# Kernel optimization log

Measured on AMD Instinct MI355X. Metric: run time of the kernel, lower is better.

## Reference

```python
import jax, jax.numpy as jnp
import numpy as np

B, V, H = 4, 256, 128
EPS = 1e-5


def setup_inputs() -> dict:
    key = jax.random.key(0)
    ks = jax.random.split(key, 16)
    inp = {
        "h1": jax.random.normal(ks[0], (B, V, H), jnp.float32),
        "h2": jax.random.normal(ks[1], (B, V, H), jnp.float32),
        "e": jax.random.normal(ks[2], (B, V, V, H), jnp.float32),
        "graph": jax.random.randint(ks[3], (B, V, V), 0, 2, jnp.int32),
    }
    scale = 1.0 / np.sqrt(H)
    for i, nm in enumerate(["U1", "U2", "V1", "V2", "A1", "A2", "C"]):
        inp[f"W_{nm}"] = jax.random.normal(ks[4 + i], (H, H), jnp.float32) * scale
        inp[f"b_{nm}"] = jnp.zeros((H,), jnp.float32)
    for nm in ["h1", "h2", "e"]:
        inp[f"g_{nm}"] = jnp.ones((H,), jnp.float32)   # BN gamma
        inp[f"be_{nm}"] = jnp.zeros((H,), jnp.float32)  # BN beta
    return inp


def _lin(x, W, b):
    # torch nn.Linear: x @ W.T + b
    return jnp.einsum('...i,oi->...o', x, W) + b


def _bn(x, g, b):
    # BatchNorm1d with track_running_stats=False: batch stats over flattened leading dims
    sh = x.shape
    x2 = x.reshape(-1, sh[-1])
    m = x2.mean(axis=0)
    v = x2.var(axis=0)  # biased, as torch BN uses for normalization
    return ((x2 - m) * jax.lax.rsqrt(v + EPS) * g + b).reshape(sh)


def reference(h1, h2, e, graph,
              W_U1, b_U1, W_U2, b_U2, W_V1, b_V1, W_V2, b_V2,
              W_A1, b_A1, W_A2, b_A2, W_C, b_C,
              g_h1, be_h1, g_h2, be_h2, g_e, be_e):
    h1_in, h2_in, e_in = h1, h2, e

    Uh1 = _lin(h1, W_U1, b_U1)
    Uh2 = _lin(h2, W_U2, b_U2)
    Vh1 = _lin(h1, W_V1, b_V1)
    Vh2 = _lin(h2, W_V2, b_V2)

    # Wh1[b,i,j,h] = Vh1[b,j,h] + Vh2[b,i,h] ; Wh2 = transpose(1,2) pattern
    Wh1 = Vh1[:, None, :, :] + Vh2[:, :, None, :]
    Wh2 = Vh1[:, :, None, :] + Vh2[:, None, :, :]

    Ah1 = _lin(h1, W_A1, b_A1)
    Ah2 = _lin(h2, W_A2, b_A2)
    Ce = _lin(e, W_C, b_C)
    e_new = Ah1[:, None, :, :] + Ah2[:, :, None, :] + Ce  # B x V x V x H

    gates = jax.nn.sigmoid(e_new)
    gates_T = jax.nn.sigmoid(jnp.transpose(e_new, (0, 2, 1, 3)))

    # aggregation = 'sum' over dim 2 (graph unused for sum)
    h1n = Uh1 + jnp.sum(gates * Wh1, axis=2)
    h2n = Uh2 + jnp.sum(gates_T * Wh2, axis=2)

    h1n = jax.nn.relu(_bn(h1n, g_h1, be_h1))
    h2n = jax.nn.relu(_bn(h2n, g_h2, be_h2))
    e_out = jax.nn.relu(_bn(e_new, g_e, be_e))

    # mode == 'residual'
    return (h1_in + h1n, h2_in + h2n, e_in + e_out)
```

## Files before the change

### kernel.cpp

```cpp
#include <hip/hip_runtime.h>
#include <hip/hip_fp16.h>
#include <math.h>

#define BB 4
#define VV 256
#define HH 128
#define EPS 1e-5f

typedef __attribute__((ext_vector_type(8))) short short8;
typedef __attribute__((ext_vector_type(8))) __bf16 bf16x8;
typedef __attribute__((ext_vector_type(4))) float f32x4;

__device__ __forceinline__ float sigm_(float x) {
    float ex = __builtin_amdgcn_exp2f(-1.44269504f * x);
    return __builtin_amdgcn_rcpf(1.0f + ex);
}

__device__ __forceinline__ bf16x8 as_bf(short8 s) {
    union { short8 s; bf16x8 b; } u; u.s = s; return u.b;
}

__device__ __forceinline__ void split8n(const float4 x0, const float4 x1,
                                        bf16x8& hi, bf16x8& lo) {
    float xs[8] = {x0.x, x0.y, x0.z, x0.w, x1.x, x1.y, x1.z, x1.w};
    #pragma unroll
    for (int i = 0; i < 8; ++i) {
        float x = xs[i];
        __bf16 h = (__bf16)x;
        float r = x - (float)h;
        hi[i] = h;
        lo[i] = (__bf16)r;
    }
}

__global__ __launch_bounds__(256) void k0_splitW(const float* __restrict__ W_C,
                                                 short* __restrict__ Whl) {
    int t = blockIdx.x * 256 + threadIdx.x;
    int lane = t & 63;
    int grp = t >> 6;
    int kstep = grp >> 3, nsub = grp & 7;
    int n = (lane & 15) * 8 + nsub;
    int kb = kstep * 32 + ((lane >> 4) & 3) * 8;
    const float4* src = (const float4*)(W_C + (size_t)n * HH + kb);
    float4 x0 = src[0], x1 = src[1];
    bf16x8 hi, lo;
    split8n(x0, x1, hi, lo);
    union { bf16x8 b; short8 s; } uh, ul;
    uh.b = hi; ul.b = lo;
    short8* dst = (short8*)Whl;
    dst[(size_t)grp * 128 + 0 * 64 + lane] = uh.s;
    dst[(size_t)grp * 128 + 1 * 64 + lane] = ul.s;
}

struct LinArgs {
    const float* x1; const float* x2;
    const float* W[6]; const float* b[6]; const float* b2[6];
    float* out[6]; float* outf[6];
};

__global__ __launch_bounds__(128) void k1_linears(LinArgs a) {
    __shared__ float xs[2][8][HH];
    const int t = threadIdx.x;
    const int r0 = blockIdx.x * 8;
    {
        const float4* s1 = (const float4*)(a.x1 + (size_t)r0 * HH);
        const float4* s2 = (const float4*)(a.x2 + (size_t)r0 * HH);
        float4* d1 = (float4*)&xs[0][0][0];
        float4* d2 = (float4*)&xs[1][0][0];
        #pragma unroll
        for (int p = 0; p < 2; ++p) {
            d1[t + p * 128] = s1[t + p * 128];
            d2[t + p * 128] = s2[t + p * 128];
        }
    }
    __syncthreads();
    const int h = t;
    const int l15h = h >> 3, nsh = h & 7;
    for (int g = 0; g < 6; ++g) {
        const float* W = a.W[g];
        const float (*x)[HH] = (g < 3) ? xs[0] : xs[1];
        float acc[8];
        #pragma unroll
        for (int r = 0; r < 8; ++r) acc[r] = 0.f;
        const float4* Wrow = (const float4*)(W + (size_t)h * HH);
        #pragma unroll 8
        for (int kq = 0; kq < 32; ++kq) {
            float4 w4 = Wrow[kq];
            #pragma unroll
            for (int r = 0; r < 8; ++r) {
                float4 ev = *(const float4*)&x[r][kq * 4];
                acc[r] = fmaf(ev.x, w4.x, acc[r]);
                acc[r] = fmaf(ev.y, w4.y, acc[r]);
                acc[r] = fmaf(ev.z, w4.z, acc[r]);
                acc[r] = fmaf(ev.w, w4.w, acc[r]);
            }
        }
        float bias = a.b[g][h];
        if (a.b2[g]) bias += a.b2[g][h];
        if (a.out[g]) {
            float* O = a.out[g] + (size_t)r0 * HH + h;
            #pragma unroll
            for (int r = 0; r < 8; ++r) O[(size_t)r * HH] = acc[r] + bias;
        }
        if (a.outf[g]) {
            float* Of = a.outf[g];
            #pragma unroll
            for (int r = 0; r < 8; ++r)
                Of[((size_t)(r0 + r) * 16 + l15h) * 8 + nsh] = acc[r] + bias;
        }
    }
}

template<int STOREH>
__global__ __launch_bounds__(512, 4) void k2_main(
    const float* __restrict__ e,
    const short* __restrict__ Whl,
    const float* __restrict__ A1f, const float* __restrict__ A2f,
    const float* __restrict__ V1f, const float* __restrict__ V2f,
    float* __restrict__ e_new32,
    unsigned short* __restrict__ e_newh,
    float* __restrict__ h1acc,
    float* __restrict__ stats)
{
    __shared__ short8 sW[4096];
    __shared__ float red[8][3][8][16];
    const int t = threadIdx.x;
    const int l = t & 63;
    const int w = t >> 6;
    const int l15 = l & 15;
    const int lq = (l >> 4) & 3;
    const int bi = blockIdx.x;
    const int b = bi >> 8;
    const int jbase = w * 32;

    {
        const short8* src = (const short8*)Whl;
        #pragma unroll
        for (int p = 0; p < 8; ++p) sW[p * 512 + t] = src[p * 512 + t];
    }
    __syncthreads();

    const float* ebase = e + (size_t)bi * (VV * HH);
    const float* pa = ebase + (size_t)(jbase + l15) * HH + lq * 8;

    f32x4 acc[2][8];
    #pragma unroll
    for (int js = 0; js < 2; ++js)
        #pragma unroll
        for (int ns = 0; ns < 8; ++ns)
            acc[js][ns] = (f32x4){0.f, 0.f, 0.f, 0.f};

    float4 ec0 = *(const float4*)(pa);
    float4 ec1 = *(const float4*)(pa + 4);
    float4 ec2 = *(const float4*)(pa + 16 * HH);
    float4 ec3 = *(const float4*)(pa + 16 * HH + 4);

    #pragma unroll
    for (int kstep = 0; kstep < 4; ++kstep) {
        bf16x8 ah[2], al[2];
        split8n(ec0, ec1, ah[0], al[0]);
        split8n(ec2, ec3, ah[1], al[1]);
        if (kstep < 3) {
            const float* pn = pa + (kstep + 1) * 32;
            ec0 = *(const float4*)(pn);
            ec1 = *(const float4*)(pn + 4);
            ec2 = *(const float4*)(pn + 16 * HH);
            ec3 = *(const float4*)(pn + 16 * HH + 4);
        }
        #pragma unroll
        for (int ns = 0; ns < 8; ++ns) {
            short8 bh = sW[(size_t)(kstep * 8 + ns) * 128 + l];
            short8 bl = sW[(size_t)(kstep * 8 + ns) * 128 + 64 + l];
            acc[0][ns] = __builtin_amdgcn_mfma_f32_16x16x32_bf16(
                ah[0], as_bf(bh), acc[0][ns], 0, 0, 0);
            acc[1][ns] = __builtin_amdgcn_mfma_f32_16x16x32_bf16(
                ah[1], as_bf(bh), acc[1][ns], 0, 0, 0);
            acc[0][ns] = __builtin_amdgcn_mfma_f32_16x16x32_bf16(
                ah[0], as_bf(bl), acc[0][ns], 0, 0, 0);
            acc[1][ns] = __builtin_amdgcn_mfma_f32_16x16x32_bf16(
                ah[1], as_bf(bl), acc[1][ns], 0, 0, 0);
            acc[0][ns] = __builtin_amdgcn_mfma_f32_16x16x32_bf16(
                al[0], as_bf(bh), acc[0][ns], 0, 0, 0);
            acc[1][ns] = __builtin_amdgcn_mfma_f32_16x16x32_bf16(
                al[1], as_bf(bh), acc[1][ns], 0, 0, 0);
        }
    }

    union f8u { float4 v[2]; float f[8]; };
    f8u a2, v2;
    {
        const float4* p = (const float4*)(A2f + ((size_t)bi * 16 + l15) * 8);
        a2.v[0] = p[0]; a2.v[1] = p[1];
        const float4* q = (const float4*)(V2f + ((size_t)bi * 16 + l15) * 8);
        v2.v[0] = q[0]; v2.v[1] = q[1];
    }
    float h1a[8], es[8], eq[8];
    #pragma unroll
    for (int ns = 0; ns < 8; ++ns) { h1a[ns] = 0.f; es[ns] = 0.f; eq[ns] = 0.f; }

    #pragma unroll
    for (int js = 0; js < 2; ++js) {
        #pragma unroll
        for (int r = 0; r < 4; ++r) {
            int j = jbase + js * 16 + lq * 4 + r;
            size_t fro = ((size_t)(b * VV + j) * 16 + l15) * 8;
            f8u a1, v1;
            {
                const float4* p = (const float4*)(A1f + fro);
                a1.v[0] = p[0]; a1.v[1] = p[1];
                const float4* q = (const float4*)(V1f + fro);
                v1.v[0] = q[0]; v1.v[1] = q[1];
            }
            size_t obase = ((size_t)bi * VV + j) * HH + l15 * 8;
            float en8[8];
            #pragma unroll
            for (int ns = 0; ns < 8; ++ns) {
                float en = acc[js][ns][r] + a1.f[ns] + a2.f[ns];
                en8[ns] = en;
                float s = sigm_(en);
                h1a[ns] = fmaf(s, v1.f[ns] + v2.f[ns], h1a[ns]);
                es[ns] += en;
                eq[ns] = fmaf(en, en, eq[ns]);
            }
            if (STOREH) {
                union { __half2 h[4]; uint4 u; } pk;
                pk.h[0] = __floats2half2_rn(en8[0], en8[1]);
                pk.h[1] = __floats2half2_rn(en8[2], en8[3]);
                pk.h[2] = __floats2half2_rn(en8[4], en8[5]);
                pk.h[3] = __floats2half2_rn(en8[6], en8[7]);
                *(uint4*)(e_newh + obase) = pk.u;
            } else {
                float4 s0 = {en8[0], en8[1], en8[2], en8[3]};
                float4 s1 = {en8[4], en8[5], en8[6], en8[7]};
                *(float4*)(e_new32 + obase) = s0;
                *(float4*)(e_new32 + obase + 4) = s1;
            }
        }
    }

    #pragma unroll
    for (int ns = 0; ns < 8; ++ns) {
        h1a[ns] += __shfl_xor(h1a[ns], 16);
        h1a[ns] += __shfl_xor(h1a[ns], 32);
        es[ns]  += __shfl_xor(es[ns], 16);
        es[ns]  += __shfl_xor(es[ns], 32);
        eq[ns]  += __shfl_xor(eq[ns], 16);
        eq[ns]  += __shfl_xor(eq[ns], 32);
    }
    if (l < 16) {
        #pragma unroll
        for (int ns = 0; ns < 8; ++ns) {
            red[w][0][ns][l15] = h1a[ns];
            red[w][1][ns][l15] = es[ns];
            red[w][2][ns][l15] = eq[ns];
        }
    }
    __syncthreads();
    if (t < 128) {
        int ns = t & 7, li = t >> 3;
        float h1t = 0.f, est = 0.f, eqt = 0.f;
        #pragma unroll
        for (int ww = 0; ww < 8; ++ww) {
            h1t += red[ww][0][ns][li];
            est += red[ww][1][ns][li];
            eqt += red[ww][2][ns][li];
        }
        h1acc[(size_t)bi * HH + t] = h1t;
        atomicAdd(&stats[0 * HH + t], est);
        atomicAdd(&stats[1 * HH + t], eqt);
    }
}

template<int READH>
__global__ __launch_bounds__(256) void k4_pass2(
    float* __restrict__ e_io,
    const unsigned short* __restrict__ e_newh,
    const float* __restrict__ e_in,
    const float* __restrict__ V1, const float* __restrict__ V2,
    const float* __restrict__ g_e, const float* __restrict__ be_e,
    float* __restrict__ h2acc,
    const float* __restrict__ stats)
{
    const int t = threadIdx.x;
    const int h4 = (t & 31) * 4;
    const int jsub = t >> 5;
    const int blk = blockIdx.x;
    const int Iq = blk & 7;
    const int Jt = (blk >> 3) & 31;
    const int b = blk >> 8;
    const int J = Jt * 8 + jsub;
    const int bJ = (b << 8) + J;

    const float inv_n = 1.0f / (float)(BB * VV * VV);
    float sc[4], sh[4];
    #pragma unroll
    for (int c = 0; c < 4; ++c) {
        int h = h4 + c;
        float mean = stats[0 * HH + h] * inv_n;
        float var  = stats[1 * HH + h] * inv_n - mean * mean;
        float rstd = rsqrtf(var + EPS);
        sc[c] = rstd * g_e[h];
        sh[c] = be_e[h] - mean * sc[c];
    }
    float4 vh1 = *(const float4*)(V1 + (size_t)bJ * HH + h4);
    float4 h2a = {0.f, 0.f, 0.f, 0.f};

    const int I0beg = Iq * 32;
    for (int I0 = I0beg; I0 < I0beg + 32; I0 += 4) {
        float4 en[4], ei[4], v2[4];
        size_t off[4];
        #pragma unroll
        for (int u = 0; u < 4; ++u) {
            int I = I0 + u;
            off[u] = ((size_t)((b * VV + I) * VV) + J) * HH + h4;
            if (READH) {
                ushort4 eh = *(const ushort4*)(e_newh + off[u]);
                en[u].x = __half2float(__ushort_as_half(eh.x));
                en[u].y = __half2float(__ushort_as_half(eh.y));
                en[u].z = __half2float(__ushort_as_half(eh.z));
                en[u].w = __half2float(__ushort_as_half(eh.w));
            } else {
                en[u] = *(const float4*)(e_io + off[u]);
            }
            ei[u] = *(const float4*)(e_in + off[u]);
            v2[u] = *(const float4*)(V2 + (size_t)((b << 8) + I) * HH + h4);
        }
        #pragma unroll
        for (int u = 0; u < 4; ++u) {
            float4 r;
            float* enf = (float*)&en[u];
            float* eif = (float*)&ei[u];
            float* v2f = (float*)&v2[u];
            float* rf = (float*)&r;
            float* h2f = (float*)&h2a;
            float* v1f = (float*)&vh1;
            #pragma unroll
            for (int c = 0; c < 4; ++c) {
                float e_ = enf[c];
                h2f[c] = fmaf(sigm_(e_), v1f[c] + v2f[c], h2f[c]);
                float bn = fmaf(e_, sc[c], sh[c]);
                rf[c] = eif[c] + fmaxf(bn, 0.f);
            }
            *(float4*)(e_io + off[u]) = r;
        }
    }
    float* base = h2acc + (size_t)bJ * HH + h4;
    float* h2f = (float*)&h2a;
    #pragma unroll
    for (int c = 0; c < 4; ++c) atomicAdd(base + c, h2f[c]);
}

__global__ __launch_bounds__(256) void k45_combine(
    float* __restrict__ h1acc, float* __restrict__ h2acc,
    const float* __restrict__ U1, const float* __restrict__ U2,
    float* __restrict__ stats)
{
    __shared__ float red[2][2][128];
    const int t = threadIdx.x;
    const int h = t & 127;
    const int rr = t >> 7;
    const int region = blockIdx.x >> 5;
    const int r0 = (blockIdx.x & 31) * 32;
    float* acc = region ? h2acc : h1acc;
    const float* U = region ? U2 : U1;
    float s = 0.f, q = 0.f;
    #pragma unroll
    for (int rs = 0; rs < 16; ++rs) {
        size_t idx = (size_t)(r0 + rr * 16 + rs) * HH + h;
        float v = acc[idx] + U[idx];
        acc[idx] = v;
        s += v;
        q = fmaf(v, v, q);
    }
    red[0][rr][h] = s;
    red[1][rr][h] = q;
    __syncthreads();
    if (t < 128) {
        atomicAdd(&stats[(2 + 2 * region) * HH + h], red[0][0][h] + red[0][1][h]);
        atomicAdd(&stats[(3 + 2 * region) * HH + h], red[1][0][h] + red[1][1][h]);
    }
}

__global__ __launch_bounds__(256) void k5_final(
    const float* __restrict__ h1_in, const float* __restrict__ h2_in,
    const float* __restrict__ h1p, const float* __restrict__ h2p,
    const float* __restrict__ g1, const float* __restrict__ be1,
    const float* __restrict__ g2, const float* __restrict__ be2,
    float* __restrict__ out,
    const float* __restrict__ stats)
{
    const float inv_n = 1.0f / 1024.0f;
    int idx0 = blockIdx.x * 2048 + threadIdx.x;
    #pragma unroll
    for (int p = 0; p < 8; ++p) {
        int idx = idx0 + p * 256;
        int region = idx >> 17;
        int local = idx & 131071;
        int h = idx & 127;
        float ssum = stats[(2 + 2 * region) * HH + h];
        float ssq  = stats[(3 + 2 * region) * HH + h];
        float mean = ssum * inv_n;
        float var  = ssq * inv_n - mean * mean;
        float rstd = rsqrtf(var + EPS);
        const float* g  = region ? g2 : g1;
        const float* be = region ? be2 : be1;
        float sc = rstd * g[h];
        float sh = be[h] - mean * sc;
        const float* xin = region ? h2_in : h1_in;
        const float* pre = region ? h2p : h1p;
        out[idx] = xin[local] + fmaxf(fmaf(pre[local], sc, sh), 0.f);
    }
}

extern "C" void kernel_launch(void* const* d_in, const int* in_sizes, int n_in,
                              void* d_out, int out_size, void* d_ws, size_t ws_size,
                              hipStream_t stream) {
    const float* h1   = (const float*)d_in[0];
    const float* h2   = (const float*)d_in[1];
    const float* e    = (const float*)d_in[2];
    const float* W_U1 = (const float*)d_in[4];
    const float* b_U1 = (const float*)d_in[5];
    const float* W_U2 = (const float*)d_in[6];
    const float* b_U2 = (const float*)d_in[7];
    const float* W_V1 = (const float*)d_in[8];
    const float* b_V1 = (const float*)d_in[9];
    const float* W_V2 = (const float*)d_in[10];
    const float* b_V2 = (const float*)d_in[11];
    const float* W_A1 = (const float*)d_in[12];
    const float* b_A1 = (const float*)d_in[13];
    const float* W_A2 = (const float*)d_in[14];
    const float* b_A2 = (const float*)d_in[15];
    const float* W_C  = (const float*)d_in[16];
    const float* b_C  = (const float*)d_in[17];
    const float* g_h1 = (const float*)d_in[18];
    const float* be_h1= (const float*)d_in[19];
    const float* g_h2 = (const float*)d_in[20];
    const float* be_h2= (const float*)d_in[21];
    const float* g_e  = (const float*)d_in[22];
    const float* be_e = (const float*)d_in[23];

    float* ws = (float*)d_ws;
    const size_t S = (size_t)BB * VV * HH;
    float* U1  = ws + 0 * S;
    float* U2  = ws + 1 * S;
    float* V1  = ws + 2 * S;
    float* V2  = ws + 3 * S;
    float* V1f = ws + 4 * S;
    float* V2f = ws + 5 * S;
    float* A1f = ws + 6 * S;
    float* A2f = ws + 7 * S;
    float* h1acc = ws + 8 * S;
    float* h2acc = ws + 9 * S;
    float* stats = ws + 10 * S;
    short* Whl  = (short*)(stats + 768);
    unsigned short* e_newh = (unsigned short*)(Whl + 32768);

    const size_t EN = (size_t)BB * VV * VV * HH;
    const size_t needed = (10 * S + 768) * 4 + 65536 + EN * 2;
    const bool useh = ws_size >= needed;

    float* out = (float*)d_out;
    float* eo = out + 2 * S;

    hipMemsetAsync(h2acc, 0, (S + 768) * sizeof(float), stream);

    k0_splitW<<<8, 256, 0, stream>>>(W_C, Whl);

    LinArgs la;
    la.x1 = h1; la.x2 = h2;
    la.W[0] = W_U1; la.b[0] = b_U1; la.b2[0] = nullptr; la.out[0] = U1; la.outf[0] = nullptr;
    la.W[1] = W_V1; la.b[1] = b_V1; la.b2[1] = nullptr; la.out[1] = V1; la.outf[1] = V1f;
    la.W[2] = W_A1; la.b[2] = b_A1; la.b2[2] = b_C;     la.out[2] = nullptr; la.outf[2] = A1f;
    la.W[3] = W_U2; la.b[3] = b_U2; la.b2[3] = nullptr; la.out[3] = U2; la.outf[3] = nullptr;
    la.W[4] = W_V2; la.b[4] = b_V2; la.b2[4] = nullptr; la.out[4] = V2; la.outf[4] = V2f;
    la.W[5] = W_A2; la.b[5] = b_A2; la.b2[5] = nullptr; la.out[5] = nullptr; la.outf[5] = A2f;
    k1_linears<<<128, 128, 0, stream>>>(la);

    if (useh) {
        k2_main<1><<<BB * VV, 512, 0, stream>>>(e, Whl, A1f, A2f, V1f, V2f,
                                                eo, e_newh, h1acc, stats);
        k4_pass2<1><<<BB * 32 * 8, 256, 0, stream>>>(eo, e_newh, e, V1, V2,
                                                     g_e, be_e, h2acc, stats);
    } else {
        k2_main<0><<<BB * VV, 512, 0, stream>>>(e, Whl, A1f, A2f, V1f, V2f,
                                                eo, e_newh, h1acc, stats);
        k4_pass2<0><<<BB * 32 * 8, 256, 0, stream>>>(eo, e_newh, e, V1, V2,
                                                     g_e, be_e, h2acc, stats);
    }

    k45_combine<<<64, 256, 0, stream>>>(h1acc, h2acc, U1, U2, stats);

    k5_final<<<128, 256, 0, stream>>>(h1, h2, h1acc, h2acc,
                                      g_h1, be_h1, g_h2, be_h2, out, stats);
}
```

Measured before the change: 180.2 us.

## Split main edge kernel over j-halves and halve linear-kernel row tiles

```diff
diff --git a/kernel.cpp b/kernel.cpp
--- a/kernel.cpp
+++ b/kernel.cpp
@@ -59,19 +59,14 @@
 };
 
 __global__ __launch_bounds__(128) void k1_linears(LinArgs a) {
-    __shared__ float xs[2][8][HH];
+    __shared__ float xs[2][4][HH];
     const int t = threadIdx.x;
-    const int r0 = blockIdx.x * 8;
+    const int r0 = blockIdx.x * 4;
     {
         const float4* s1 = (const float4*)(a.x1 + (size_t)r0 * HH);
         const float4* s2 = (const float4*)(a.x2 + (size_t)r0 * HH);
-        float4* d1 = (float4*)&xs[0][0][0];
-        float4* d2 = (float4*)&xs[1][0][0];
-        #pragma unroll
-        for (int p = 0; p < 2; ++p) {
-            d1[t + p * 128] = s1[t + p * 128];
-            d2[t + p * 128] = s2[t + p * 128];
-        }
+        ((float4*)&xs[0][0][0])[t] = s1[t];
+        ((float4*)&xs[1][0][0])[t] = s2[t];
     }
     __syncthreads();
     const int h = t;
@@ -79,15 +74,15 @@
     for (int g = 0; g < 6; ++g) {
         const float* W = a.W[g];
         const float (*x)[HH] = (g < 3) ? xs[0] : xs[1];
-        float acc[8];
-        #pragma unroll
-        for (int r = 0; r < 8; ++r) acc[r] = 0.f;
+        float acc[4];
+        #pragma unroll
+        for (int r = 0; r < 4; ++r) acc[r] = 0.f;
         const float4* Wrow = (const float4*)(W + (size_t)h * HH);
         #pragma unroll 8
         for (int kq = 0; kq < 32; ++kq) {
             float4 w4 = Wrow[kq];
             #pragma unroll
-            for (int r = 0; r < 8; ++r) {
+            for (int r = 0; r < 4; ++r) {
                 float4 ev = *(const float4*)&x[r][kq * 4];
                 acc[r] = fmaf(ev.x, w4.x, acc[r]);
                 acc[r] = fmaf(ev.y, w4.y, acc[r]);
@@ -100,12 +95,12 @@
         if (a.out[g]) {
             float* O = a.out[g] + (size_t)r0 * HH + h;
             #pragma unroll
-            for (int r = 0; r < 8; ++r) O[(size_t)r * HH] = acc[r] + bias;
+            for (int r = 0; r < 4; ++r) O[(size_t)r * HH] = acc[r] + bias;
         }
         if (a.outf[g]) {
             float* Of = a.outf[g];
             #pragma unroll
-            for (int r = 0; r < 8; ++r)
+            for (int r = 0; r < 4; ++r)
                 Of[((size_t)(r0 + r) * 16 + l15h) * 8 + nsh] = acc[r] + bias;
         }
     }
@@ -129,9 +124,11 @@
     const int w = t >> 6;
     const int l15 = l & 15;
     const int lq = (l >> 4) & 3;
-    const int bi = blockIdx.x;
+    const int blk = blockIdx.x;
+    const int bi = blk >> 1;
+    const int jhalf = blk & 1;
     const int b = bi >> 8;
-    const int jbase = w * 32;
+    const int jbase = jhalf * 128 + w * 16;
 
     {
         const short8* src = (const short8*)Whl;
@@ -140,49 +137,35 @@
     }
     __syncthreads();
 
-    const float* ebase = e + (size_t)bi * (VV * HH);
-    const float* pa = ebase + (size_t)(jbase + l15) * HH + lq * 8;
-
-    f32x4 acc[2][8];
-    #pragma unroll
-    for (int js = 0; js < 2; ++js)
-        #pragma unroll
-        for (int ns = 0; ns < 8; ++ns)
-            acc[js][ns] = (f32x4){0.f, 0.f, 0.f, 0.f};
+    const float* pa = e + (size_t)bi * (VV * HH) +
+                      (size_t)(jbase + l15) * HH + lq * 8;
+
+    f32x4 acc[8];
+    #pragma unroll
+    for (int ns = 0; ns < 8; ++ns) acc[ns] = (f32x4){0.f, 0.f, 0.f, 0.f};
 
     float4 ec0 = *(const float4*)(pa);
     float4 ec1 = *(const float4*)(pa + 4);
-    float4 ec2 = *(const float4*)(pa + 16 * HH);
-    float4 ec3 = *(const float4*)(pa + 16 * HH + 4);
 
     #pragma unroll
     for (int kstep = 0; kstep < 4; ++kstep) {
-        bf16x8 ah[2], al[2];
-        split8n(ec0, ec1, ah[0], al[0]);
-        split8n(ec2, ec3, ah[1], al[1]);
+        bf16x8 ah, al;
+        split8n(ec0, ec1, ah, al);
         if (kstep < 3) {
             const float* pn = pa + (kstep + 1) * 32;
             ec0 = *(const float4*)(pn);
             ec1 = *(const float4*)(pn + 4);
-            ec2 = *(const float4*)(pn + 16 * HH);
-            ec3 = *(const float4*)(pn + 16 * HH + 4);
         }
         #pragma unroll
         for (int ns = 0; ns < 8; ++ns) {
             short8 bh = sW[(size_t)(kstep * 8 + ns) * 128 + l];
             short8 bl = sW[(size_t)(kstep * 8 + ns) * 128 + 64 + l];
-            acc[0][ns] = __builtin_amdgcn_mfma_f32_16x16x32_bf16(
-                ah[0], as_bf(bh), acc[0][ns], 0, 0, 0);
-            acc[1][ns] = __builtin_amdgcn_mfma_f32_16x16x32_bf16(
-                ah[1], as_bf(bh), acc[1][ns], 0, 0, 0);
-            acc[0][ns] = __builtin_amdgcn_mfma_f32_16x16x32_bf16(
-                ah[0], as_bf(bl), acc[0][ns], 0, 0, 0);
-            acc[1][ns] = __builtin_amdgcn_mfma_f32_16x16x32_bf16(
-                ah[1], as_bf(bl), acc[1][ns], 0, 0, 0);
-            acc[0][ns] = __builtin_amdgcn_mfma_f32_16x16x32_bf16(
-                al[0], as_bf(bh), acc[0][ns], 0, 0, 0);
-            acc[1][ns] = __builtin_amdgcn_mfma_f32_16x16x32_bf16(
-                al[1], as_bf(bh), acc[1][ns], 0, 0, 0);
+            acc[ns] = __builtin_amdgcn_mfma_f32_16x16x32_bf16(
+                ah, as_bf(bh), acc[ns], 0, 0, 0);
+            acc[ns] = __builtin_amdgcn_mfma_f32_16x16x32_bf16(
+                ah, as_bf(bl), acc[ns], 0, 0, 0);
+            acc[ns] = __builtin_amdgcn_mfma_f32_16x16x32_bf16(
+                al, as_bf(bh), acc[ns], 0, 0, 0);
         }
     }
 
@@ -199,42 +182,39 @@
     for (int ns = 0; ns < 8; ++ns) { h1a[ns] = 0.f; es[ns] = 0.f; eq[ns] = 0.f; }
 
     #pragma unroll
-    for (int js = 0; js < 2; ++js) {
-        #pragma unroll
-        for (int r = 0; r < 4; ++r) {
-            int j = jbase + js * 16 + lq * 4 + r;
-            size_t fro = ((size_t)(b * VV + j) * 16 + l15) * 8;
-            f8u a1, v1;
-            {
-                const float4* p = (const float4*)(A1f + fro);
-                a1.v[0] = p[0]; a1.v[1] = p[1];
-                const float4* q = (const float4*)(V1f + fro);
-                v1.v[0] = q[0]; v1.v[1] = q[1];
-            }
-            size_t obase = ((size_t)bi * VV + j) * HH + l15 * 8;
-            float en8[8];
-            #pragma unroll
-            for (int ns = 0; ns < 8; ++ns) {
-                float en = acc[js][ns][r] + a1.f[ns] + a2.f[ns];
-                en8[ns] = en;
-                float s = sigm_(en);
-                h1a[ns] = fmaf(s, v1.f[ns] + v2.f[ns], h1a[ns]);
-                es[ns] += en;
-                eq[ns] = fmaf(en, en, eq[ns]);
-            }
-            if (STOREH) {
-                union { __half2 h[4]; uint4 u; } pk;
-                pk.h[0] = __floats2half2_rn(en8[0], en8[1]);
-                pk.h[1] = __floats2half2_rn(en8[2], en8[3]);
-                pk.h[2] = __floats2half2_rn(en8[4], en8[5]);
-                pk.h[3] = __floats2half2_rn(en8[6], en8[7]);
-                *(uint4*)(e_newh + obase) = pk.u;
-            } else {
-                float4 s0 = {en8[0], en8[1], en8[2], en8[3]};
-                float4 s1 = {en8[4], en8[5], en8[6], en8[7]};
-                *(float4*)(e_new32 + obase) = s0;
-                *(float4*)(e_new32 + obase + 4) = s1;
-            }
+    for (int r = 0; r < 4; ++r) {
+        int j = jbase + lq * 4 + r;
+        size_t fro = ((size_t)(b * VV + j) * 16 + l15) * 8;
+        f8u a1, v1;
+        {
+            const float4* p = (const float4*)(A1f + fro);
+            a1.v[0] = p[0]; a1.v[1] = p[1];
+            const float4* q = (const float4*)(V1f + fro);
+            v1.v[0] = q[0]; v1.v[1] = q[1];
+        }
+        size_t obase = ((size_t)bi * VV + j) * HH + l15 * 8;
+        float en8[8];
+        #pragma unroll
+        for (int ns = 0; ns < 8; ++ns) {
+            float en = acc[ns][r] + a1.f[ns] + a2.f[ns];
+            en8[ns] = en;
+            float s = sigm_(en);
+            h1a[ns] = fmaf(s, v1.f[ns] + v2.f[ns], h1a[ns]);
+            es[ns] += en;
+            eq[ns] = fmaf(en, en, eq[ns]);
+        }
+        if (STOREH) {
+            union { __half2 h[4]; uint4 u; } pk;
+            pk.h[0] = __floats2half2_rn(en8[0], en8[1]);
+            pk.h[1] = __floats2half2_rn(en8[2], en8[3]);
+            pk.h[2] = __floats2half2_rn(en8[4], en8[5]);
+            pk.h[3] = __floats2half2_rn(en8[6], en8[7]);
+            *(uint4*)(e_newh + obase) = pk.u;
+        } else {
+            float4 s0 = {en8[0], en8[1], en8[2], en8[3]};
+            float4 s1 = {en8[4], en8[5], en8[6], en8[7]};
+            *(float4*)(e_new32 + obase) = s0;
+            *(float4*)(e_new32 + obase + 4) = s1;
         }
     }
 
@@ -265,7 +245,7 @@
             est += red[ww][1][ns][li];
             eqt += red[ww][2][ns][li];
         }
-        h1acc[(size_t)bi * HH + t] = h1t;
+        atomicAdd(&h1acc[(size_t)bi * HH + t], h1t);
         atomicAdd(&stats[0 * HH + t], est);
         atomicAdd(&stats[1 * HH + t], eqt);
     }
@@ -462,7 +442,7 @@
     float* out = (float*)d_out;
     float* eo = out + 2 * S;
 
-    hipMemsetAsync(h2acc, 0, (S + 768) * sizeof(float), stream);
+    hipMemsetAsync(h1acc, 0, (2 * S + 768) * sizeof(float), stream);
 
     k0_splitW<<<8, 256, 0, stream>>>(W_C, Whl);
 
@@ -474,16 +454,16 @@
     la.W[3] = W_U2; la.b[3] = b_U2; la.b2[3] = nullptr; la.out[3] = U2; la.outf[3] = nullptr;
     la.W[4] = W_V2; la.b[4] = b_V2; la.b2[4] = nullptr; la.out[4] = V2; la.outf[4] = V2f;
     la.W[5] = W_A2; la.b[5] = b_A2; la.b2[5] = nullptr; la.out[5] = nullptr; la.outf[5] = A2f;
-    k1_linears<<<128, 128, 0, stream>>>(la);
+    k1_linears<<<256, 128, 0, stream>>>(la);
 
     if (useh) {
-        k2_main<1><<<BB * VV, 512, 0, stream>>>(e, Whl, A1f, A2f, V1f, V2f,
-                                                eo, e_newh, h1acc, stats);
+        k2_main<1><<<BB * VV * 2, 512, 0, stream>>>(e, Whl, A1f, A2f, V1f, V2f,
+                                                    eo, e_newh, h1acc, stats);
         k4_pass2<1><<<BB * 32 * 8, 256, 0, stream>>>(eo, e_newh, e, V1, V2,
                                                      g_e, be_e, h2acc, stats);
     } else {
-        k2_main<0><<<BB * VV, 512, 0, stream>>>(e, Whl, A1f, A2f, V1f, V2f,
-                                                eo, e_newh, h1acc, stats);
+        k2_main<0><<<BB * VV * 2, 512, 0, stream>>>(e, Whl, A1f, A2f, V1f, V2f,
+                                                    eo, e_newh, h1acc, stats);
         k4_pass2<0><<<BB * 32 * 8, 256, 0, stream>>>(eo, e_newh, e, V1, V2,
                                                      g_e, be_e, h2acc, stats);
     }
```

Measured after the change: 194.4 us. +7.9%, slower.
